# Kernel tuning notes

Hardware: AMD Instinct MI355X
Metric: run time of the kernel (lower is better)

Reference implementation:

```python
import jax, jax.numpy as jnp
import numpy as np

D_MODEL = 1024
N_TILES = 16
BATCH = 32768
THRESH = 0.3


def setup_inputs() -> dict:
    key = jax.random.key(0)
    k_x, k_sig, k_w, k_b = jax.random.split(key, 4)
    x = jax.random.normal(k_x, (BATCH, D_MODEL), dtype=jnp.float32)
    # nn.Parameter(torch.randn(n_tiles, d_model) * 0.5)
    signatures_raw = jax.random.normal(k_sig, (N_TILES, D_MODEL), dtype=jnp.float32) * 0.5
    # nn.Linear(d_model, d_model) default init: U(-1/sqrt(fan_in), 1/sqrt(fan_in))
    bound = 1.0 / np.sqrt(D_MODEL)
    W = jax.random.uniform(k_w, (N_TILES, D_MODEL, D_MODEL), dtype=jnp.float32, minval=-bound, maxval=bound)
    b = jax.random.uniform(k_b, (N_TILES, D_MODEL), dtype=jnp.float32, minval=-bound, maxval=bound)
    return {"x": x, "signatures_raw": signatures_raw, "W": W, "b": b}


def _quantize_ternary(s):
    # straight-through ternary: forward value is q, gradient is identity
    q = jnp.where(s > THRESH, 1.0, jnp.where(s < -THRESH, -1.0, 0.0))
    return s + jax.lax.stop_gradient(q - s)


def reference(x, signatures_raw, W, b):
    sigs = _quantize_ternary(signatures_raw)          # [E, D]
    scores = x @ sigs.T                               # [B, E]
    tile_indices = jnp.argmax(scores, axis=-1)        # [B]
    out = jnp.zeros_like(x)
    # fixed small loop over experts: masked combine of per-expert Linear+ReLU
    for e in range(N_TILES):
        y = jax.nn.relu(x @ W[e].T + b[e])            # [B, D]
        out = out + jnp.where((tile_indices == e)[:, None], y, 0.0)
    out = out + x                                     # residual
    return out, tile_indices
```

## Files before the change

### kernel.cpp

```cpp
#include <hip/hip_runtime.h>
#include <hip/hip_bf16.h>

#define BATCH   32768
#define DM      1024
#define NE      16
#define THRESHF 0.3f
#define MARGIN  0.02f

#define CTRL_OFF 131072
#define QBF_OFF  139264
#define PERM_OFF 172032
#define XBF_OFF  319488
#define WB_OFF   67428352ull
#define WS_NEED  (WB_OFF + (size_t)NE * DM * DM * 2)

typedef __attribute__((ext_vector_type(8))) short bf16x8;
typedef __attribute__((ext_vector_type(4))) float f32x4;

#define MFMA16(a, b, c) __builtin_amdgcn_mfma_f32_16x16x32_bf16(a, b, c, 0, 0, 0)

static __device__ __forceinline__ unsigned short f2bf(float f) {
    union { float f; unsigned u; } v; v.f = f;
    unsigned r = (v.u + 0x7FFFu + ((v.u >> 16) & 1u)) >> 16;
    return (unsigned short)r;
}
static __device__ __forceinline__ float bf2f(unsigned short h) {
    union { unsigned u; float f; } v; v.u = ((unsigned)h) << 16;
    return v.f;
}

static __device__ __forceinline__ void gload_lds16(const void* g, void* s) {
    __builtin_amdgcn_global_load_lds(
        (const __attribute__((address_space(1))) void*)g,
        (__attribute__((address_space(3))) void*)s, 16, 0, 0);
}

static __device__ __forceinline__ int tile_base(const unsigned* ctrl, int* tb) {
    int acc = 0;
#pragma unroll
    for (int e = 0; e < NE; ++e) {
        tb[e] = acc;
        acc += (int)((ctrl[e * 16] + 127u) >> 7);
    }
    tb[NE] = acc;
    return acc;
}

__global__ void k_init(const float* __restrict__ sig, unsigned* __restrict__ ctrl,
                       int* __restrict__ perm, unsigned short* __restrict__ Qbf) {
    const int t = blockIdx.x * 256 + threadIdx.x;
    if (t < 544) ctrl[t] = 0;
    if (t < 1024) {
        unsigned pm = 0, mm = 0;
#pragma unroll
        for (int e = 0; e < NE; ++e) {
            float s = sig[e * DM + t];
            pm |= (s > THRESHF ? 1u : 0u) << e;
            mm |= (s < -THRESHF ? 1u : 0u) << e;
        }
        ctrl[1024 + t] = pm | (mm << 16);
    }
    if (t < 9216) ((int4*)perm)[t] = make_int4(0, 0, 0, 0);
    {
        float s = sig[t];
        Qbf[t] = s > THRESHF ? (unsigned short)0x3F80u
                             : (s < -THRESHF ? (unsigned short)0xBF80u : (unsigned short)0u);
    }
}

__global__ __launch_bounds__(256) void k_router(const float* __restrict__ x,
                                                const unsigned short* __restrict__ Qbf,
                                                unsigned* __restrict__ ctrl,
                                                int* __restrict__ idx,
                                                float* __restrict__ outIdx,
                                                unsigned short* __restrict__ Xbf,
                                                int writeXbf) {
    __shared__ float S[4][64][4];
    const int t = threadIdx.x, w = t >> 6, l = t & 63;
    const int lc = l & 15, lr = l >> 4;
    const int row0 = blockIdx.x * 16;
    const unsigned* packT = ctrl + 1024;

    const float* ax = x + (size_t)(row0 + lc) * DM + lr * 8;
    const unsigned short* qx = Qbf + (size_t)lc * DM + lr * 8;
    unsigned short* xb = Xbf + (size_t)(row0 + lc) * DM + lr * 8;

    f32x4 acc = (f32x4){0.f, 0.f, 0.f, 0.f};

    for (int kt = w * 4; kt < w * 4 + 4; ++kt) {
#pragma unroll
        for (int h = 0; h < 2; ++h) {
            const int ko = kt * 64 + h * 32;
            float4 v0 = *(const float4*)(ax + ko);
            float4 v1 = *(const float4*)(ax + ko + 4);
            bf16x8 q = *(const bf16x8*)(qx + ko);

            float f[8] = {v0.x, v0.y, v0.z, v0.w, v1.x, v1.y, v1.z, v1.w};
            bf16x8 ah, al;
#pragma unroll
            for (int j = 0; j < 8; ++j) {
                unsigned short hi = f2bf(f[j]);
                float r = f[j] - bf2f(hi);
                ah[j] = (short)hi;
                al[j] = (short)f2bf(r);
            }
            if (writeXbf) *(bf16x8*)(xb + ko) = ah;
            acc = MFMA16(ah, q, acc);
            acc = MFMA16(al, q, acc);
        }
    }

    *(f32x4*)&S[w][l][0] = acc;
    __syncthreads();
    if (w != 0) return;

#pragma unroll
    for (int s = 1; s < 4; ++s) acc += *(const f32x4*)&S[s][l][0];

    float bv[4]; int bi[4]; float gap[4];
#pragma unroll
    for (int reg = 0; reg < 4; ++reg) {
        float v = acc[reg]; int i = lc; float s = -3.4e38f;
#pragma unroll
        for (int m = 1; m < 16; m <<= 1) {
            float ov = __shfl_xor(v, m, 64);
            int oi = __shfl_xor(i, m, 64);
            float os = __shfl_xor(s, m, 64);
            bool take = (ov > v) || (ov == v && oi < i);
            float loser = take ? v : ov;
            v = take ? ov : v;
            i = take ? oi : i;
            s = fmaxf(fmaxf(s, os), loser);
        }
        bv[reg] = v; bi[reg] = i; gap[reg] = v - s;
    }

    unsigned flagsw = 0;
#pragma unroll
    for (int reg = 0; reg < 4; ++reg)
        flagsw |= (gap[reg] < MARGIN ? 1u : 0u) << reg;

    if (__any(lc == 0 && flagsw != 0)) {
#pragma unroll
        for (int reg = 0; reg < 4; ++reg) {
            for (int g = 0; g < 4; ++g) {
                const unsigned fw = __shfl(flagsw, g * 16, 64);
                if ((fw >> reg) & 1u) {
                    const int row = row0 + g * 4 + reg;
                    const float* xr = x + (size_t)row * DM;
                    float xv[16]; unsigned mk[16];
#pragma unroll
                    for (int k2 = 0; k2 < 16; ++k2) {
                        xv[k2] = xr[k2 * 64 + l];
                        mk[k2] = packT[k2 * 64 + l];
                    }
                    double best = 0.0; int bbi = 0;
                    for (int e = 0; e < 16; ++e) {
                        double a = 0.0;
#pragma unroll
                        for (int k2 = 0; k2 < 16; ++k2) {
                            const int pb = (int)((mk[k2] >> e) & 1u);
                            const int mb = (int)((mk[k2] >> (16 + e)) & 1u);
                            a += pb ? (double)xv[k2] : (mb ? -(double)xv[k2] : 0.0);
                        }
#pragma unroll
                        for (int m = 1; m < 64; m <<= 1) a += __shfl_xor(a, m, 64);
                        if (e == 0 || a > best) { best = a; bbi = e; }
                    }
                    if (lr == g && lc == 0) bi[reg] = bbi;
                }
            }
        }
    }

    if (lc == 0) {
#pragma unroll
        for (int reg = 0; reg < 4; ++reg) {
            const int row = row0 + lr * 4 + reg;
            idx[row] = bi[reg];
            outIdx[row] = (float)bi[reg];
            atomicAdd(&ctrl[bi[reg] * 16], 1u);
        }
    }
}

__global__ __launch_bounds__(256) void k_permconv(const int* __restrict__ idx,
                                                  unsigned* __restrict__ ctrl,
                                                  int* __restrict__ perm,
                                                  const float* __restrict__ W,
                                                  unsigned short* __restrict__ Wb) {
    if (blockIdx.x >= 128) {
        const size_t g = ((size_t)(blockIdx.x - 128) * 256 + threadIdx.x) * 8;
        float4 a = *(const float4*)&W[g];
        float4 b = *(const float4*)&W[g + 4];
        *(ushort4*)&Wb[g]     = make_ushort4(f2bf(a.x), f2bf(a.y), f2bf(a.z), f2bf(a.w));
        *(ushort4*)&Wb[g + 4] = make_ushort4(f2bf(b.x), f2bf(b.y), f2bf(b.z), f2bf(b.w));
        return;
    }
    __shared__ unsigned hcnt[16];
    __shared__ unsigned hbase[16];
    const int t = threadIdx.x;
    const int row = blockIdx.x * 256 + t;
    int tb[NE + 1];
    tile_base(ctrl, tb);
    if (t < 16) hcnt[t] = 0;
    __syncthreads();
    const int e = idx[row];
    const unsigned lrank = atomicAdd(&hcnt[e], 1u);
    __syncthreads();
    if (t < 16) hbase[t] = atomicAdd(&ctrl[256 + t * 16], hcnt[t]);
    __syncthreads();
    perm[tb[e] * 128 + hbase[e] + lrank] = row;
}

__global__ __launch_bounds__(256) void k_gemm(
        const unsigned short* __restrict__ Xbf,
        const unsigned short* __restrict__ Wb,
        const float* __restrict__ bias,
        const int* __restrict__ perm,
        const unsigned* __restrict__ ctrl,
        float* __restrict__ out) {
    __shared__ unsigned short A_lds[3][128 * 32];
    __shared__ unsigned short B_lds[3][128 * 32];

    int tb[NE + 1];
    const int total = tile_base(ctrl, tb);

    int bx, ny;
    {
        const int flat = blockIdx.x;
        const int xcd = flat & 7, s2 = flat >> 3;
        bx = xcd * 34 + (s2 >> 3);
        ny = s2 & 7;
    }
    if (bx >= total) return;
    int e = 0;
    while (e < NE - 1 && tb[e + 1] <= bx) ++e;
    const int valid = (int)ctrl[e * 16] - (bx - tb[e]) * 128;
    const int n0 = ny * 128;

    const int t = threadIdx.x, w = t >> 6, l = t & 63;
    const int wr = w >> 1, wc = w & 1;
    const int lc = l & 15, lr = l >> 4;
    const int hsw = ((t & 3) - ((t >> 3) & 3)) & 3;
    const int ssw = (lr + (lc >> 1)) & 3;

    f32x4 acc[4][4];
#pragma unroll
    for (int m = 0; m < 4; ++m)
#pragma unroll
        for (int n = 0; n < 4; ++n) acc[m][n] = (f32x4){0.f, 0.f, 0.f, 0.f};

    const size_t aRowBase = (size_t)bx * 128;
    const unsigned short* Bg = Wb + ((size_t)e * DM + n0) * DM;

    const int r0 = t >> 2;
    const int prow0 = perm[aRowBase + r0];
    const int prow1 = perm[aRowBase + 64 + r0];
    const unsigned short* a0 = Xbf + (size_t)prow0 * DM + hsw * 8;
    const unsigned short* a1 = Xbf + (size_t)prow1 * DM + hsw * 8;
    const unsigned short* b0 = Bg + (size_t)r0 * DM + hsw * 8;
    const unsigned short* b1 = Bg + (size_t)(64 + r0) * DM + hsw * 8;

    auto STAGE = [&](int kt, int buf) {
        const int ko = kt * 32;
        gload_lds16(a0 + ko, &A_lds[buf][(size_t)(w * 64) * 8]);
        gload_lds16(a1 + ko, &A_lds[buf][(size_t)(256 + w * 64) * 8]);
        gload_lds16(b0 + ko, &B_lds[buf][(size_t)(w * 64) * 8]);
        gload_lds16(b1 + ko, &B_lds[buf][(size_t)(256 + w * 64) * 8]);
    };

    STAGE(0, 0);
    STAGE(1, 1);

    const int NT = DM / 32;
    int cur = 0;
    for (int kt = 0; kt < NT; ++kt) {
        if (kt + 1 < NT) asm volatile("s_waitcnt vmcnt(4)" ::: "memory");
        else             asm volatile("s_waitcnt vmcnt(0)" ::: "memory");
        __builtin_amdgcn_sched_barrier(0);
        __builtin_amdgcn_s_barrier();
        __builtin_amdgcn_sched_barrier(0);

        if (kt + 2 < NT) {
            const int nb = (cur + 2 >= 3) ? cur - 1 : cur + 2;
            STAGE(kt + 2, nb);
        }

        bf16x8 af[4], bf[4];
#pragma unroll
        for (int m = 0; m < 4; ++m)
            af[m] = *(const bf16x8*)&A_lds[cur][(wr * 64 + m * 16 + lc) * 32 + ssw * 8];
#pragma unroll
        for (int n = 0; n < 4; ++n)
            bf[n] = *(const bf16x8*)&B_lds[cur][(wc * 64 + n * 16 + lc) * 32 + ssw * 8];
#pragma unroll
        for (int m = 0; m < 4; ++m)
#pragma unroll
            for (int n = 0; n < 4; ++n)
                acc[m][n] = MFMA16(af[m], bf[n], acc[m][n]);

        cur = (cur + 1 >= 3) ? 0 : cur + 1;
    }

    float bvv[4];
#pragma unroll
    for (int n = 0; n < 4; ++n) bvv[n] = bias[e * DM + n0 + wc * 64 + n * 16 + lc];

#pragma unroll
    for (int m = 0; m < 4; ++m) {
#pragma unroll
        for (int reg = 0; reg < 4; ++reg) {
            const int rit = wr * 64 + m * 16 + lr * 4 + reg;
            if (rit < valid) {
                const int orow = perm[aRowBase + rit];
                float* op = out + (size_t)orow * DM;
                const unsigned short* xr = Xbf + (size_t)orow * DM;
#pragma unroll
                for (int n = 0; n < 4; ++n) {
                    const int col = n0 + wc * 64 + n * 16 + lc;
                    float v = acc[m][n][reg] + bvv[n];
                    v = v > 0.f ? v : 0.f;
                    op[col] = v + bf2f(xr[col]);
                }
            }
        }
    }
}

__global__ __launch_bounds__(256) void k_gemm_small(
        const float* __restrict__ x, const float* __restrict__ W,
        const float* __restrict__ bias, const int* __restrict__ perm,
        const unsigned* __restrict__ ctrl, float* __restrict__ out) {
    __shared__ unsigned short A_lds[128 * 32];
    __shared__ unsigned short B_lds[128 * 32];
    int tb[NE + 1];
    const int total = tile_base(ctrl, tb);
    int bx, ny;
    {
        const int flat = blockIdx.x;
        const int xcd = flat & 7, s2 = flat >> 3;
        bx = xcd * 34 + (s2 >> 3);
        ny = s2 & 7;
    }
    if (bx >= total) return;
    int e = 0;
    while (e < NE - 1 && tb[e + 1] <= bx) ++e;
    const int valid = (int)ctrl[e * 16] - (bx - tb[e]) * 128;
    const int n0 = ny * 128;
    const int t = threadIdx.x, w = t >> 6, l = t & 63;
    const int wr = w >> 1, wc = w & 1;
    const int lc = l & 15, lr = l >> 4;
    const int hsw = ((t & 3) - ((t >> 3) & 3)) & 3;
    const int ssw = (lr + (lc >> 1)) & 3;

    f32x4 acc[4][4];
#pragma unroll
    for (int m = 0; m < 4; ++m)
#pragma unroll
        for (int n = 0; n < 4; ++n) acc[m][n] = (f32x4){0.f, 0.f, 0.f, 0.f};
    const size_t aRowBase = (size_t)bx * 128;

    for (int kt = 0; kt < DM / 32; ++kt) {
        __syncthreads();
#pragma unroll
        for (int rd = 0; rd < 2; ++rd) {
            const int c = rd * 256 + t;
            const int r = c >> 2;
            const float* wp = W + ((size_t)e * DM + n0 + r) * DM + kt * 32 + hsw * 8;
            float4 q0 = *(const float4*)wp;
            float4 q1 = *(const float4*)(wp + 4);
            *(ushort4*)&B_lds[c * 8]     = make_ushort4(f2bf(q0.x), f2bf(q0.y), f2bf(q0.z), f2bf(q0.w));
            *(ushort4*)&B_lds[c * 8 + 4] = make_ushort4(f2bf(q1.x), f2bf(q1.y), f2bf(q1.z), f2bf(q1.w));
            ushort4 p0 = make_ushort4(0, 0, 0, 0), p1 = p0;
            if (r < valid) {
                const int orow = perm[aRowBase + r];
                const float* xp = x + (size_t)orow * DM + kt * 32 + hsw * 8;
                float4 u0 = *(const float4*)xp;
                float4 u1 = *(const float4*)(xp + 4);
                p0 = make_ushort4(f2bf(u0.x), f2bf(u0.y), f2bf(u0.z), f2bf(u0.w));
                p1 = make_ushort4(f2bf(u1.x), f2bf(u1.y), f2bf(u1.z), f2bf(u1.w));
            }
            *(ushort4*)&A_lds[c * 8]     = p0;
            *(ushort4*)&A_lds[c * 8 + 4] = p1;
        }
        __syncthreads();
        bf16x8 af[4], bf[4];
#pragma unroll
        for (int m = 0; m < 4; ++m)
            af[m] = *(const bf16x8*)&A_lds[(wr * 64 + m * 16 + lc) * 32 + ssw * 8];
#pragma unroll
        for (int n = 0; n < 4; ++n)
            bf[n] = *(const bf16x8*)&B_lds[(wc * 64 + n * 16 + lc) * 32 + ssw * 8];
#pragma unroll
        for (int m = 0; m < 4; ++m)
#pragma unroll
            for (int n = 0; n < 4; ++n)
                acc[m][n] = MFMA16(af[m], bf[n], acc[m][n]);
    }

    float bvv[4];
#pragma unroll
    for (int n = 0; n < 4; ++n) bvv[n] = bias[e * DM + n0 + wc * 64 + n * 16 + lc];
#pragma unroll
    for (int m = 0; m < 4; ++m)
#pragma unroll
        for (int reg = 0; reg < 4; ++reg) {
            const int rit = wr * 64 + m * 16 + lr * 4 + reg;
            if (rit < valid) {
                const int orow = perm[aRowBase + rit];
                const float* xr = x + (size_t)orow * DM;
                float* op = out + (size_t)orow * DM;
#pragma unroll
                for (int n = 0; n < 4; ++n) {
                    const int col = n0 + wc * 64 + n * 16 + lc;
                    float v = acc[m][n][reg] + bvv[n];
                    v = v > 0.f ? v : 0.f;
                    op[col] = v + xr[col];
                }
            }
        }
}

extern "C" void kernel_launch(void* const* d_in, const int* in_sizes, int n_in,
                              void* d_out, int out_size, void* d_ws, size_t ws_size,
                              hipStream_t stream) {
    const float* x    = (const float*)d_in[0];
    const float* sig  = (const float*)d_in[1];
    const float* W    = (const float*)d_in[2];
    const float* bias = (const float*)d_in[3];
    float* out = (float*)d_out;
    float* outIdx = out + (size_t)BATCH * DM;

    char* ws = (char*)d_ws;
    int* idx = (int*)ws;
    unsigned* ctrl = (unsigned*)(ws + CTRL_OFF);
    unsigned short* Qbf = (unsigned short*)(ws + QBF_OFF);
    int* perm = (int*)(ws + PERM_OFF);
    unsigned short* Xbf = (unsigned short*)(ws + XBF_OFF);
    unsigned short* Wb = (unsigned short*)(ws + WB_OFF);

    const bool full = ws_size >= WS_NEED;

    k_init<<<64, 256, 0, stream>>>(sig, ctrl, perm, Qbf);
    k_router<<<2048, 256, 0, stream>>>(x, Qbf, ctrl, idx, outIdx, Xbf, full ? 1 : 0);
    k_permconv<<<full ? 8320 : 128, 256, 0, stream>>>(idx, ctrl, perm, W, Wb);
    if (full) {
        k_gemm<<<2176, 256, 0, stream>>>(Xbf, Wb, bias, perm, ctrl, out);
    } else {
        k_gemm_small<<<2176, 256, 0, stream>>>(x, W, bias, perm, ctrl, out);
    }
}
```

Before: 221.2 us.

## Switch expert GEMM from bf16 to fp8 with scaled weights

```diff
diff --git a/kernel.cpp b/kernel.cpp
--- a/kernel.cpp
+++ b/kernel.cpp
@@ -10,14 +10,15 @@
 #define CTRL_OFF 131072
 #define QBF_OFF  139264
 #define PERM_OFF 172032
-#define XBF_OFF  319488
-#define WB_OFF   67428352ull
-#define WS_NEED  (WB_OFF + (size_t)NE * DM * DM * 2)
+#define X8_OFF   319488
+#define W8_OFF   33873920ull
+#define WS_NEED  (W8_OFF + (size_t)NE * DM * DM)
 
 typedef __attribute__((ext_vector_type(8))) short bf16x8;
 typedef __attribute__((ext_vector_type(4))) float f32x4;
 
-#define MFMA16(a, b, c) __builtin_amdgcn_mfma_f32_16x16x32_bf16(a, b, c, 0, 0, 0)
+#define MFMA16(a, b, c)  __builtin_amdgcn_mfma_f32_16x16x32_bf16(a, b, c, 0, 0, 0)
+#define MFMAF8(a, b, c)  __builtin_amdgcn_mfma_f32_16x16x32_fp8_fp8(a, b, c, 0, 0, 0)
 
 static __device__ __forceinline__ unsigned short f2bf(float f) {
     union { float f; unsigned u; } v; v.f = f;
@@ -27,6 +28,22 @@
 static __device__ __forceinline__ float bf2f(unsigned short h) {
     union { unsigned u; float f; } v; v.u = ((unsigned)h) << 16;
     return v.f;
+}
+
+static __device__ __forceinline__ unsigned f2fp8(float f) {
+    union { float f; unsigned u; } v; v.f = f;
+    const unsigned s = (v.u >> 24) & 0x80u;
+    const float a = __builtin_fabsf(f);
+    if (a >= 448.0f) return s | 0x7Eu;
+    if (a < 0.015625f) {
+        const int n = (int)rintf(a * 512.0f);
+        return s | (unsigned)n;
+    }
+    unsigned u = v.u;
+    u += 0x7FFFFu + ((u >> 20) & 1u);
+    const int e = (int)((u >> 23) & 0xFF) - 127;
+    const unsigned m = (u >> 20) & 7u;
+    return s | ((unsigned)(e + 7) << 3) | m;
 }
 
 static __device__ __forceinline__ void gload_lds16(const void* g, void* s) {
@@ -73,8 +90,8 @@
                                                 unsigned* __restrict__ ctrl,
                                                 int* __restrict__ idx,
                                                 float* __restrict__ outIdx,
-                                                unsigned short* __restrict__ Xbf,
-                                                int writeXbf) {
+                                                unsigned char* __restrict__ X8,
+                                                int writeX8) {
     __shared__ float S[4][64][4];
     const int t = threadIdx.x, w = t >> 6, l = t & 63;
     const int lc = l & 15, lr = l >> 4;
@@ -83,7 +100,7 @@
 
     const float* ax = x + (size_t)(row0 + lc) * DM + lr * 8;
     const unsigned short* qx = Qbf + (size_t)lc * DM + lr * 8;
-    unsigned short* xb = Xbf + (size_t)(row0 + lc) * DM + lr * 8;
+    unsigned char* xb = X8 + (size_t)(row0 + lc) * DM + lr * 8;
 
     f32x4 acc = (f32x4){0.f, 0.f, 0.f, 0.f};
 
@@ -97,14 +114,16 @@
 
             float f[8] = {v0.x, v0.y, v0.z, v0.w, v1.x, v1.y, v1.z, v1.w};
             bf16x8 ah, al;
+            unsigned long long p8 = 0ull;
 #pragma unroll
             for (int j = 0; j < 8; ++j) {
                 unsigned short hi = f2bf(f[j]);
                 float r = f[j] - bf2f(hi);
                 ah[j] = (short)hi;
                 al[j] = (short)f2bf(r);
-            }
-            if (writeXbf) *(bf16x8*)(xb + ko) = ah;
+                p8 |= (unsigned long long)f2fp8(f[j]) << (8 * j);
+            }
+            if (writeX8) *(unsigned long long*)(xb + ko) = p8;
             acc = MFMA16(ah, q, acc);
             acc = MFMA16(al, q, acc);
         }
@@ -188,13 +207,17 @@
                                                   unsigned* __restrict__ ctrl,
                                                   int* __restrict__ perm,
                                                   const float* __restrict__ W,
-                                                  unsigned short* __restrict__ Wb) {
+                                                  unsigned char* __restrict__ W8) {
     if (blockIdx.x >= 128) {
         const size_t g = ((size_t)(blockIdx.x - 128) * 256 + threadIdx.x) * 8;
         float4 a = *(const float4*)&W[g];
         float4 b = *(const float4*)&W[g + 4];
-        *(ushort4*)&Wb[g]     = make_ushort4(f2bf(a.x), f2bf(a.y), f2bf(a.z), f2bf(a.w));
-        *(ushort4*)&Wb[g + 4] = make_ushort4(f2bf(b.x), f2bf(b.y), f2bf(b.z), f2bf(b.w));
+        float f[8] = {a.x, a.y, a.z, a.w, b.x, b.y, b.z, b.w};
+        unsigned long long p8 = 0ull;
+#pragma unroll
+        for (int j = 0; j < 8; ++j)
+            p8 |= (unsigned long long)f2fp8(f[j] * 16.0f) << (8 * j);
+        *(unsigned long long*)(W8 + g) = p8;
         return;
     }
     __shared__ unsigned hcnt[16];
@@ -214,14 +237,15 @@
 }
 
 __global__ __launch_bounds__(256) void k_gemm(
-        const unsigned short* __restrict__ Xbf,
-        const unsigned short* __restrict__ Wb,
+        const unsigned char* __restrict__ X8,
+        const unsigned char* __restrict__ W8,
         const float* __restrict__ bias,
         const int* __restrict__ perm,
         const unsigned* __restrict__ ctrl,
+        const float* __restrict__ x,
         float* __restrict__ out) {
-    __shared__ unsigned short A_lds[3][128 * 32];
-    __shared__ unsigned short B_lds[3][128 * 32];
+    __shared__ unsigned char A_lds[3][8192];
+    __shared__ unsigned char B_lds[3][8192];
 
     int tb[NE + 1];
     const int total = tile_base(ctrl, tb);
@@ -243,7 +267,7 @@
     const int wr = w >> 1, wc = w & 1;
     const int lc = l & 15, lr = l >> 4;
     const int hsw = ((t & 3) - ((t >> 3) & 3)) & 3;
-    const int ssw = (lr + (lc >> 1)) & 3;
+    const int d4b = lr >> 1, off8 = (lr & 1) * 8;
 
     f32x4 acc[4][4];
 #pragma unroll
@@ -252,28 +276,28 @@
         for (int n = 0; n < 4; ++n) acc[m][n] = (f32x4){0.f, 0.f, 0.f, 0.f};
 
     const size_t aRowBase = (size_t)bx * 128;
-    const unsigned short* Bg = Wb + ((size_t)e * DM + n0) * DM;
+    const unsigned char* Bg = W8 + ((size_t)e * DM + n0) * DM;
 
     const int r0 = t >> 2;
     const int prow0 = perm[aRowBase + r0];
     const int prow1 = perm[aRowBase + 64 + r0];
-    const unsigned short* a0 = Xbf + (size_t)prow0 * DM + hsw * 8;
-    const unsigned short* a1 = Xbf + (size_t)prow1 * DM + hsw * 8;
-    const unsigned short* b0 = Bg + (size_t)r0 * DM + hsw * 8;
-    const unsigned short* b1 = Bg + (size_t)(64 + r0) * DM + hsw * 8;
+    const unsigned char* a0 = X8 + (size_t)prow0 * DM + hsw * 16;
+    const unsigned char* a1 = X8 + (size_t)prow1 * DM + hsw * 16;
+    const unsigned char* b0 = Bg + (size_t)r0 * DM + hsw * 16;
+    const unsigned char* b1 = Bg + (size_t)(64 + r0) * DM + hsw * 16;
 
     auto STAGE = [&](int kt, int buf) {
-        const int ko = kt * 32;
-        gload_lds16(a0 + ko, &A_lds[buf][(size_t)(w * 64) * 8]);
-        gload_lds16(a1 + ko, &A_lds[buf][(size_t)(256 + w * 64) * 8]);
-        gload_lds16(b0 + ko, &B_lds[buf][(size_t)(w * 64) * 8]);
-        gload_lds16(b1 + ko, &B_lds[buf][(size_t)(256 + w * 64) * 8]);
+        const int ko = kt * 64;
+        gload_lds16(a0 + ko, &A_lds[buf][w * 1024]);
+        gload_lds16(a1 + ko, &A_lds[buf][4096 + w * 1024]);
+        gload_lds16(b0 + ko, &B_lds[buf][w * 1024]);
+        gload_lds16(b1 + ko, &B_lds[buf][4096 + w * 1024]);
     };
 
     STAGE(0, 0);
     STAGE(1, 1);
 
-    const int NT = DM / 32;
+    const int NT = DM / 64;
     int cur = 0;
     for (int kt = 0; kt < NT; ++kt) {
         if (kt + 1 < NT) asm volatile("s_waitcnt vmcnt(4)" ::: "memory");
@@ -287,18 +311,27 @@
             STAGE(kt + 2, nb);
         }
 
-        bf16x8 af[4], bf[4];
-#pragma unroll
-        for (int m = 0; m < 4; ++m)
-            af[m] = *(const bf16x8*)&A_lds[cur][(wr * 64 + m * 16 + lc) * 32 + ssw * 8];
-#pragma unroll
-        for (int n = 0; n < 4; ++n)
-            bf[n] = *(const bf16x8*)&B_lds[cur][(wc * 64 + n * 16 + lc) * 32 + ssw * 8];
-#pragma unroll
-        for (int m = 0; m < 4; ++m)
-#pragma unroll
-            for (int n = 0; n < 4; ++n)
-                acc[m][n] = MFMA16(af[m], bf[n], acc[m][n]);
+#pragma unroll
+        for (int ks = 0; ks < 2; ++ks) {
+            long af[4], bf[4];
+#pragma unroll
+            for (int m = 0; m < 4; ++m) {
+                const int r = wr * 64 + m * 16 + lc;
+                af[m] = *(const long*)&A_lds[cur][r * 64 +
+                        (((ks * 2 + d4b) + ((r >> 1) & 3)) & 3) * 16 + off8];
+            }
+#pragma unroll
+            for (int n = 0; n < 4; ++n) {
+                const int r = wc * 64 + n * 16 + lc;
+                bf[n] = *(const long*)&B_lds[cur][r * 64 +
+                        (((ks * 2 + d4b) + ((r >> 1) & 3)) & 3) * 16 + off8];
+            }
+#pragma unroll
+            for (int m = 0; m < 4; ++m)
+#pragma unroll
+                for (int n = 0; n < 4; ++n)
+                    acc[m][n] = MFMAF8(af[m], bf[n], acc[m][n]);
+        }
 
         cur = (cur + 1 >= 3) ? 0 : cur + 1;
     }
@@ -315,13 +348,13 @@
             if (rit < valid) {
                 const int orow = perm[aRowBase + rit];
                 float* op = out + (size_t)orow * DM;
-                const unsigned short* xr = Xbf + (size_t)orow * DM;
+                const float* xr = x + (size_t)orow * DM;
 #pragma unroll
                 for (int n = 0; n < 4; ++n) {
                     const int col = n0 + wc * 64 + n * 16 + lc;
-                    float v = acc[m][n][reg] + bvv[n];
+                    float v = acc[m][n][reg] * 0.0625f + bvv[n];
                     v = v > 0.f ? v : 0.f;
-                    op[col] = v + bf2f(xr[col]);
+                    op[col] = v + xr[col];
                 }
             }
         }
@@ -437,16 +470,16 @@
     unsigned* ctrl = (unsigned*)(ws + CTRL_OFF);
     unsigned short* Qbf = (unsigned short*)(ws + QBF_OFF);
     int* perm = (int*)(ws + PERM_OFF);
-    unsigned short* Xbf = (unsigned short*)(ws + XBF_OFF);
-    unsigned short* Wb = (unsigned short*)(ws + WB_OFF);
+    unsigned char* X8 = (unsigned char*)(ws + X8_OFF);
+    unsigned char* W8 = (unsigned char*)(ws + W8_OFF);
 
     const bool full = ws_size >= WS_NEED;
 
     k_init<<<64, 256, 0, stream>>>(sig, ctrl, perm, Qbf);
-    k_router<<<2048, 256, 0, stream>>>(x, Qbf, ctrl, idx, outIdx, Xbf, full ? 1 : 0);
-    k_permconv<<<full ? 8320 : 128, 256, 0, stream>>>(idx, ctrl, perm, W, Wb);
+    k_router<<<2048, 256, 0, stream>>>(x, Qbf, ctrl, idx, outIdx, X8, full ? 1 : 0);
+    k_permconv<<<full ? 8320 : 128, 256, 0, stream>>>(idx, ctrl, perm, W, W8);
     if (full) {
-        k_gemm<<<2176, 256, 0, stream>>>(Xbf, Wb, bias, perm, ctrl, out);
+        k_gemm<<<2176, 256, 0, stream>>>(X8, W8, bias, perm, ctrl, x, out);
     } else {
         k_gemm_small<<<2176, 256, 0, stream>>>(x, W, bias, perm, ctrl, out);
     }
```

Measured after the change: 223.6 us. Within noise of the previous version (+1.1%).
